# Performance work log

Measured on AMD Instinct MI355X. Metric: run time of the kernel, lower is better.

## Reference

```python
import jax, jax.numpy as jnp
import numpy as np

B, H, T, D = 2, 16, 2048, 64


def setup_inputs() -> dict:
    key = jax.random.key(0)
    kq, kk, kv, km = jax.random.split(key, 4)
    q = jax.random.normal(kq, (B, H, T, D), dtype=jnp.float32)
    k = jax.random.normal(kk, (B, H, T, D), dtype=jnp.float32)
    v = jax.random.normal(kv, (B, H, T, D), dtype=jnp.float32)
    # boolean mask, True = masked out (broadcast over batch and heads)
    mask = jax.random.randint(km, (1, 1, T, T), 0, 2).astype(jnp.bool_)
    return {"q": q, "k": k, "v": v, "mask": mask}


def reference(q, k, v, mask):
    scale = q.shape[-1] ** (-0.5)
    # [B,H,T,T] score matrix (materialized, as in the original)
    scores = jnp.einsum("bhqd,bhkd->bhqk", q, k) * scale
    scores = jnp.where(mask, jnp.float32(-10000.0), scores)
    attn = jax.nn.softmax(scores, axis=-1)
    attn = jnp.where(mask, jnp.float32(0.0), attn)
    return jnp.einsum("bhqk,bhkd->bhqd", attn, v)
```

## Files before the change

### kernel.cpp

```cpp
#include <hip/hip_runtime.h>
#include <hip/hip_bf16.h>

typedef __bf16 bf16x8 __attribute__((ext_vector_type(8)));
typedef __bf16 bf16x4 __attribute__((ext_vector_type(4)));
typedef float  f32x4  __attribute__((ext_vector_type(4)));

#define T_SEQ 2048
#define D_HEAD 64
#define BH_N 32
#define NT_TILES (T_SEQ / 64)
#define QT_N 16
#define IMG_BYTES 16384
#define SCALE_LOG2 0.18033688011112042f

#define WS_IMG ((size_t)0)
#define WS_MB  ((size_t)16u << 20)

static __device__ __forceinline__ f32x4 mfma32(bf16x8 a, bf16x8 b, f32x4 c) {
    return __builtin_amdgcn_mfma_f32_16x16x32_bf16(a, b, c, 0, 0, 0);
}

static __device__ __forceinline__ float fast_exp2(float x) {
#if __has_builtin(__builtin_amdgcn_exp2f)
    return __builtin_amdgcn_exp2f(x);
#else
    return exp2f(x);
#endif
}

static __device__ __forceinline__ void gload16(const void* g, void* l, int lane) {
#if __has_builtin(__builtin_amdgcn_global_load_lds)
    (void)lane;
    __builtin_amdgcn_global_load_lds(
        (const __attribute__((address_space(1))) void*)g,
        (__attribute__((address_space(3))) void*)l, 16, 0, 0);
#else
    *((f32x4*)l + lane) = *(const f32x4*)g;
#endif
}


__global__ __launch_bounds__(256) void prep_kv(const float* __restrict__ k,
                                               const float* __restrict__ v,
                                               char* __restrict__ img) {
    __shared__ __bf16 t[64][72];
    const int bh = blockIdx.y, tt = blockIdx.x, tid = threadIdx.x;
    char* ob = img + ((size_t)bh * NT_TILES + tt) * IMG_BYTES;
    {
        const int kr = tid >> 2, qd = tid & 3, ke = kr & 7;
        const size_t base = ((size_t)bh * T_SEQ + tt * 64 + kr) * D_HEAD + qd * 16;
        const float4 a0 = *(const float4*)(k + base);
        const float4 a1 = *(const float4*)(k + base + 4);
        const float4 a2 = *(const float4*)(k + base + 8);
        const float4 a3 = *(const float4*)(k + base + 12);
        bf16x8 w0, w1;
        w0[0]=(__bf16)a0.x; w0[1]=(__bf16)a0.y; w0[2]=(__bf16)a0.z; w0[3]=(__bf16)a0.w;
        w0[4]=(__bf16)a1.x; w0[5]=(__bf16)a1.y; w0[6]=(__bf16)a1.z; w0[7]=(__bf16)a1.w;
        w1[0]=(__bf16)a2.x; w1[1]=(__bf16)a2.y; w1[2]=(__bf16)a2.z; w1[3]=(__bf16)a2.w;
        w1[4]=(__bf16)a3.x; w1[5]=(__bf16)a3.y; w1[6]=(__bf16)a3.z; w1[7]=(__bf16)a3.w;
        *(bf16x8*)(ob + kr * 128 + (((2 * qd + 0) ^ ke) << 4)) = w0;
        *(bf16x8*)(ob + kr * 128 + (((2 * qd + 1) ^ ke) << 4)) = w1;
    }
    {
        const int tr = tid >> 4, c4 = (tid & 15) * 4;
        const float* src = v + ((size_t)bh * T_SEQ + tt * 64) * D_HEAD;
#pragma unroll
        for (int p = 0; p < 4; ++p) {
            const int row = p * 16 + tr;
            const float4 f = *(const float4*)(src + row * D_HEAD + c4);
            t[c4+0][row] = (__bf16)f.x; t[c4+1][row] = (__bf16)f.y;
            t[c4+2][row] = (__bf16)f.z; t[c4+3][row] = (__bf16)f.w;
        }
        __syncthreads();
        const int d = tid >> 2;
        char* vb = ob + 8192 + d * 128;
#pragma unroll
        for (int mi = 0; mi < 2; ++mi) {
            const int m  = (tid & 3) * 2 + mi;
            const int u  = m ^ (d & 7);
            const int k0 = (u & 1) * 32 + (u >> 1) * 4;
            const bf16x4 lo = *(const bf16x4*)&t[d][k0];
            const bf16x4 hi = *(const bf16x4*)&t[d][k0 + 16];
            *(bf16x8*)(vb + m * 16) = __builtin_shufflevector(lo, hi, 0,1,2,3,4,5,6,7);
        }
    }
}

__global__ void mpack(const int* __restrict__ m, unsigned* __restrict__ nbt) {
    const int i = blockIdx.x * 256 + threadIdx.x;
    const unsigned long long b = __ballot(m[i] != 0);
    if ((threadIdx.x & 63) == 0) {
        const int wi  = i >> 6;
        const int row = wi >> 5;
        const int t   = wi & 31;
        nbt[(size_t)(t * 2 + 0) * 2048 + row] = ~(unsigned)b;
        nbt[(size_t)(t * 2 + 1) * 2048 + row] = ~(unsigned)(b >> 32);
    }
}


__global__ __launch_bounds__(512, 4) void attn15(
    const float* __restrict__ q, const char* __restrict__ img,
    const unsigned* __restrict__ nbt, float* __restrict__ out)
{
    const int l   = blockIdx.x;
    const int m_  = l >> 3;
    const int bh  = ((l & 7) << 2) | (m_ & 3);
    const int qt  = m_ >> 2;

    const int tid = threadIdx.x, wave = tid >> 6, lane = tid & 63;
    const int g = lane >> 4, ln = lane & 15;
    const int qp = wave & 3, kh = wave >> 2;
    const int g4 = g * 4;

    __shared__ __align__(16) char smem[33280];
    float* Ep = (float*)smem;
    float* Os = (float*)(smem + 32768);

    const int qw = qt * 128 + qp * 32;

    bf16x8 qf[2][2];
#pragma unroll
    for (int qs = 0; qs < 2; ++qs) {
        const float* qpt = q + ((size_t)bh * T_SEQ + qw + qs * 16 + ln) * D_HEAD + g * 8;
#pragma unroll
        for (int kc = 0; kc < 2; ++kc) {
            const float4 f0 = *(const float4*)(qpt + kc * 32);
            const float4 f1 = *(const float4*)(qpt + kc * 32 + 4);
            qf[qs][kc][0]=(__bf16)(f0.x*SCALE_LOG2); qf[qs][kc][1]=(__bf16)(f0.y*SCALE_LOG2);
            qf[qs][kc][2]=(__bf16)(f0.z*SCALE_LOG2); qf[qs][kc][3]=(__bf16)(f0.w*SCALE_LOG2);
            qf[qs][kc][4]=(__bf16)(f1.x*SCALE_LOG2); qf[qs][kc][5]=(__bf16)(f1.y*SCALE_LOG2);
            qf[qs][kc][6]=(__bf16)(f1.z*SCALE_LOG2); qf[qs][kc][7]=(__bf16)(f1.w*SCALE_LOG2);
        }
    }

    f32x4 o[2][4];
#pragma unroll
    for (int qs = 0; qs < 2; ++qs)
#pragma unroll
        for (int mt = 0; mt < 4; ++mt) o[qs][mt] = (f32x4){0.f, 0.f, 0.f, 0.f};
    f32x4 osum[2] = { (f32x4){0.f,0.f,0.f,0.f}, (f32x4){0.f,0.f,0.f,0.f} };
    const bf16x8 ones8 = { (__bf16)1.0f, (__bf16)1.0f, (__bf16)1.0f, (__bf16)1.0f,
                           (__bf16)1.0f, (__bf16)1.0f, (__bf16)1.0f, (__bf16)1.0f };
    const f32x4 z4 = (f32x4){0.f, 0.f, 0.f, 0.f};

    const char* ibase = img + (size_t)bh * (NT_TILES * (size_t)IMG_BYTES);
    const unsigned* nb_base = nbt + (size_t)kh * 2048 + qw;

    int koffs[2][2];
#pragma unroll
    for (int ntl = 0; ntl < 2; ++ntl) {
        const int row = (2 * kh + ntl) * 16 + ln;
        const int rb = row * 128 + ((g ^ (ln & 7)) << 4);
        koffs[ntl][0] = rb; koffs[ntl][1] = rb ^ 64;
    }
    int voffs[4];
#pragma unroll
    for (int mt = 0; mt < 4; ++mt)
        voffs[mt] = (mt * 16 + ln) * 128 + ((((g << 1) | kh) ^ (ln & 7)) << 4);

    char* buf0 = smem;
    char* buf1 = smem + 16384;

    auto stage = [&](int tile, char* dstbase) {
        const char* src = ibase + (size_t)tile * IMG_BYTES + wave * 2048 + lane * 16;
        char* dst = dstbase + wave * 2048;
        gload16(src, dst, lane);
        gload16(src + 1024, dst + 1024, lane);
    };

    auto compute_tile = [&](const char* KB, const char* VB, unsigned nw0, unsigned nw1) {
        const unsigned nbs0 = nw0 >> g4;
        const unsigned nbs1 = nw1 >> g4;

        bf16x8 ka[2][2];
#pragma unroll
        for (int ntl = 0; ntl < 2; ++ntl) {
            ka[ntl][0] = *(const bf16x8*)(KB + koffs[ntl][0]);
            ka[ntl][1] = *(const bf16x8*)(KB + koffs[ntl][1]);
        }

        bf16x8 pa8[2];
#pragma unroll
        for (int ntl = 0; ntl < 2; ++ntl) {
#pragma unroll
            for (int qs = 0; qs < 2; ++qs) {
                __builtin_amdgcn_s_setprio(1);
                f32x4 c = mfma32(ka[ntl][0], qf[qs][0], z4);
                c = mfma32(ka[ntl][1], qf[qs][1], c);
                __builtin_amdgcn_s_setprio(0);
                const unsigned nbs = qs ? nbs1 : nbs0;
#pragma unroll
                for (int r = 0; r < 4; ++r) {
                    const float e = fast_exp2(c[r]);
                    const int keep = (int)(nbs << (31 - (ntl * 16 + r))) >> 31;
                    const float p = __builtin_bit_cast(float,
                        __builtin_bit_cast(unsigned, e) & (unsigned)keep);
                    pa8[qs][ntl * 4 + r] = (__bf16)p;
                }
            }
        }

        bf16x8 vv[4];
#pragma unroll
        for (int mt = 0; mt < 4; ++mt) vv[mt] = *(const bf16x8*)(VB + voffs[mt]);
        __builtin_amdgcn_s_setprio(1);
#pragma unroll
        for (int qs = 0; qs < 2; ++qs) osum[qs] = mfma32(pa8[qs], ones8, osum[qs]);
#pragma unroll
        for (int mt = 0; mt < 4; ++mt)
#pragma unroll
            for (int qs = 0; qs < 2; ++qs)
                o[qs][mt] = mfma32(pa8[qs], vv[mt], o[qs][mt]);
        __builtin_amdgcn_s_setprio(0);
    };

    stage(0, buf0);
    unsigned mwA0 = nb_base[ln], mwA1 = nb_base[16 + ln];
    __syncthreads();

#pragma unroll 1
    for (int i = 0; i < NT_TILES / 2; ++i) {
        const int t = 2 * i;
        stage(t + 1, buf1);
        const unsigned* pB = nb_base + (size_t)(t + 1) * 4096;
        const unsigned mwB0 = pB[ln], mwB1 = pB[16 + ln];
        compute_tile(buf0, buf0 + 8192, mwA0, mwA1);
        __syncthreads();
        if (i < NT_TILES / 2 - 1) {
            stage(t + 2, buf0);
            const unsigned* pA = nb_base + (size_t)(t + 2) * 4096;
            mwA0 = pA[ln]; mwA1 = pA[16 + ln];
        }
        compute_tile(buf1, buf1 + 8192, mwB0, mwB1);
        __syncthreads();
    }

#pragma unroll
    for (int pass = 0; pass < 2; ++pass) {
        if ((qp >> 1) == pass) {
            const int qpl = qp & 1;
#pragma unroll
            for (int qs = 0; qs < 2; ++qs) {
#pragma unroll
                for (int mt = 0; mt < 4; ++mt)
#pragma unroll
                    for (int r = 0; r < 4; ++r)
                        Ep[(size_t)kh * 4096 + (qpl * 32 + qs * 16 + g * 4 + r) * 64 + mt * 16 + ln] = o[qs][mt][r];
                if (ln == 0) {
#pragma unroll
                    for (int r = 0; r < 4; ++r)
                        Os[kh * 64 + qpl * 32 + qs * 16 + g * 4 + r] = osum[qs][r];
                }
            }
        }
        __syncthreads();
#pragma unroll
        for (int p2 = 0; p2 < 2; ++p2) {
            const int idx = p2 * 512 + tid;
            const int row = idx >> 4, c4 = (idx & 15) * 4;
            const float sl = Os[row] + Os[64 + row];
            const float inv = (sl > 0.f) ? (1.f / sl) : 0.f;
            const float4 a  = *(const float4*)(Ep + row * 64 + c4);
            const float4 b4 = *(const float4*)(Ep + 4096 + row * 64 + c4);
            const float4 st = { (a.x + b4.x) * inv, (a.y + b4.y) * inv,
                                (a.z + b4.z) * inv, (a.w + b4.w) * inv };
            *(float4*)(out + ((size_t)bh * T_SEQ + qt * 128 + pass * 64 + row) * D_HEAD + c4) = st;
        }
        if (pass == 0) __syncthreads();
    }
}

extern "C" void kernel_launch(void* const* d_in, const int* in_sizes, int n_in,
                              void* d_out, int out_size, void* d_ws, size_t ws_size,
                              hipStream_t stream) {
    const float* q    = (const float*)d_in[0];
    const float* k    = (const float*)d_in[1];
    const float* v    = (const float*)d_in[2];
    const int*   mask = (const int*)d_in[3];
    float*       out  = (float*)d_out;

    char* img = (char*)d_ws + WS_IMG;
    unsigned* nbt = (unsigned*)((char*)d_ws + WS_MB);

    prep_kv<<<dim3(NT_TILES, BH_N), 256, 0, stream>>>(k, v, img);
    mpack<<<(T_SEQ * T_SEQ) / 256, 256, 0, stream>>>(mask, nbt);
    attn15<<<dim3(QT_N * BH_N), 512, 0, stream>>>(q, img, nbt, out);
}
```

Baseline: 155.6 us.

## Quad-buffer K/V tiles in LDS with two tiles per barrier

Expands the LDS staging from two to four K/V tile buffers so prefetch runs two tiles ahead, and halves the number of block-wide barriers per tile. The loop is restructured into groups of four tiles with an explicit epilogue. It also replaces the shift-based mask bit extraction with a signed bitfield extract intrinsic. The doubled LDS footprint reduces how many blocks can reside per CU.

```diff
diff --git a/kernel.cpp b/kernel.cpp
--- a/kernel.cpp
+++ b/kernel.cpp
@@ -25,6 +25,14 @@
     return __builtin_amdgcn_exp2f(x);
 #else
     return exp2f(x);
+#endif
+}
+
+static __device__ __forceinline__ int sext_bit(unsigned w, int idx) {
+#if __has_builtin(__builtin_amdgcn_sbfe)
+    return __builtin_amdgcn_sbfe((int)w, idx, 1);
+#else
+    return (int)(w << (31 - idx)) >> 31;
 #endif
 }
 
@@ -99,7 +107,7 @@
 }
 
 
-__global__ __launch_bounds__(512, 4) void attn15(
+__global__ __launch_bounds__(512, 4) void attn16(
     const float* __restrict__ q, const char* __restrict__ img,
     const unsigned* __restrict__ nbt, float* __restrict__ out)
 {
@@ -113,9 +121,9 @@
     const int qp = wave & 3, kh = wave >> 2;
     const int g4 = g * 4;
 
-    __shared__ __align__(16) char smem[33280];
+    __shared__ __align__(16) char smem[66048];
     float* Ep = (float*)smem;
-    float* Os = (float*)(smem + 32768);
+    float* Os = (float*)(smem + 65536);
 
     const int qw = qt * 128 + qp * 32;
 
@@ -159,8 +167,10 @@
     for (int mt = 0; mt < 4; ++mt)
         voffs[mt] = (mt * 16 + ln) * 128 + ((((g << 1) | kh) ^ (ln & 7)) << 4);
 
-    char* buf0 = smem;
-    char* buf1 = smem + 16384;
+    char* const b0 = smem;
+    char* const b1 = smem + 16384;
+    char* const b2 = smem + 32768;
+    char* const b3 = smem + 49152;
 
     auto stage = [&](int tile, char* dstbase) {
         const char* src = ibase + (size_t)tile * IMG_BYTES + wave * 2048 + lane * 16;
@@ -169,7 +179,8 @@
         gload16(src + 1024, dst + 1024, lane);
     };
 
-    auto compute_tile = [&](const char* KB, const char* VB, unsigned nw0, unsigned nw1) {
+    auto compute_tile = [&](const char* KB, unsigned nw0, unsigned nw1) {
+        const char* VB = KB + 8192;
         const unsigned nbs0 = nw0 >> g4;
         const unsigned nbs1 = nw1 >> g4;
 
@@ -193,7 +204,7 @@
 #pragma unroll
                 for (int r = 0; r < 4; ++r) {
                     const float e = fast_exp2(c[r]);
-                    const int keep = (int)(nbs << (31 - (ntl * 16 + r))) >> 31;
+                    const int keep = sext_bit(nbs, ntl * 16 + r);
                     const float p = __builtin_bit_cast(float,
                         __builtin_bit_cast(unsigned, e) & (unsigned)keep);
                     pa8[qs][ntl * 4 + r] = (__bf16)p;
@@ -215,25 +226,64 @@
         __builtin_amdgcn_s_setprio(0);
     };
 
-    stage(0, buf0);
-    unsigned mwA0 = nb_base[ln], mwA1 = nb_base[16 + ln];
+    unsigned mwA0, mwA1, mwB0, mwB1;
+
+    stage(0, b0);
+    stage(1, b1);
+    mwA0 = nb_base[ln]; mwA1 = nb_base[16 + ln];
     __syncthreads();
 
 #pragma unroll 1
-    for (int i = 0; i < NT_TILES / 2; ++i) {
-        const int t = 2 * i;
-        stage(t + 1, buf1);
-        const unsigned* pB = nb_base + (size_t)(t + 1) * 4096;
-        const unsigned mwB0 = pB[ln], mwB1 = pB[16 + ln];
-        compute_tile(buf0, buf0 + 8192, mwA0, mwA1);
+    for (int i = 0; i < 7; ++i) {
+        const int t = 4 * i;
+        {
+            stage(t + 2, b2);
+            const unsigned* p = nb_base + (size_t)(t + 1) * 4096;
+            mwB0 = p[ln]; mwB1 = p[16 + ln];
+            compute_tile(b0, mwA0, mwA1);
+        }
+        {
+            stage(t + 3, b3);
+            const unsigned* p = nb_base + (size_t)(t + 2) * 4096;
+            mwA0 = p[ln]; mwA1 = p[16 + ln];
+            compute_tile(b1, mwB0, mwB1);
+        }
         __syncthreads();
-        if (i < NT_TILES / 2 - 1) {
-            stage(t + 2, buf0);
-            const unsigned* pA = nb_base + (size_t)(t + 2) * 4096;
-            mwA0 = pA[ln]; mwA1 = pA[16 + ln];
-        }
-        compute_tile(buf1, buf1 + 8192, mwB0, mwB1);
+        {
+            stage(t + 4, b0);
+            const unsigned* p = nb_base + (size_t)(t + 3) * 4096;
+            mwB0 = p[ln]; mwB1 = p[16 + ln];
+            compute_tile(b2, mwA0, mwA1);
+        }
+        {
+            stage(t + 5, b1);
+            const unsigned* p = nb_base + (size_t)(t + 4) * 4096;
+            mwA0 = p[ln]; mwA1 = p[16 + ln];
+            compute_tile(b3, mwB0, mwB1);
+        }
         __syncthreads();
+    }
+
+    {
+        stage(30, b2);
+        const unsigned* p = nb_base + (size_t)29 * 4096;
+        mwB0 = p[ln]; mwB1 = p[16 + ln];
+        compute_tile(b0, mwA0, mwA1);
+    }
+    {
+        stage(31, b3);
+        const unsigned* p = nb_base + (size_t)30 * 4096;
+        mwA0 = p[ln]; mwA1 = p[16 + ln];
+        compute_tile(b1, mwB0, mwB1);
+    }
+    __syncthreads();
+    {
+        const unsigned* p = nb_base + (size_t)31 * 4096;
+        mwB0 = p[ln]; mwB1 = p[16 + ln];
+        compute_tile(b2, mwA0, mwA1);
+    }
+    {
+        compute_tile(b3, mwB0, mwB1);
     }
 
 #pragma unroll
@@ -285,5 +335,5 @@
 
     prep_kv<<<dim3(NT_TILES, BH_N), 256, 0, stream>>>(k, v, img);
     mpack<<<(T_SEQ * T_SEQ) / 256, 256, 0, stream>>>(mask, nbt);
-    attn15<<<dim3(QT_N * BH_N), 512, 0, stream>>>(q, img, nbt, out);
-}
+    attn16<<<dim3(QT_N * BH_N), 512, 0, stream>>>(q, img, nbt, out);
+}
```

Measured after the change: 153.5 us, median of 2. About the same (-1.3%).

## Double per-wave query tile and deepen K/V LDS prefetch to an eight-buffer ring

Applied to the files above, without the earlier changes.

Each wave now handles 64 query rows instead of 32, so every staged K/V tile feeds twice as many MFMAs, and the grid shrinks to 256 workgroups. The two-buffer double-buffering is replaced by an eight-slot LDS ring that prefetches six tiles ahead, with one barrier per pair of tiles, to hide global-load latency. Mask bit extraction uses a signed bitfield-extract builtin. In exchange, LDS use grows to about 130 KB per block and register pressure roughly doubles, which limits occupancy to about one block per CU and halves the number of blocks available to spread across the GPU.

```diff
diff --git a/kernel.cpp b/kernel.cpp
--- a/kernel.cpp
+++ b/kernel.cpp
@@ -9,7 +9,7 @@
 #define D_HEAD 64
 #define BH_N 32
 #define NT_TILES (T_SEQ / 64)
-#define QT_N 16
+#define QT_N 8
 #define IMG_BYTES 16384
 #define SCALE_LOG2 0.18033688011112042f
 
@@ -25,6 +25,14 @@
     return __builtin_amdgcn_exp2f(x);
 #else
     return exp2f(x);
+#endif
+}
+
+static __device__ __forceinline__ int sext_bit(unsigned w, int idx) {
+#if __has_builtin(__builtin_amdgcn_sbfe)
+    return __builtin_amdgcn_sbfe((int)w, idx, 1);
+#else
+    return (int)(w << (31 - idx)) >> 31;
 #endif
 }
 
@@ -99,29 +107,28 @@
 }
 
 
-__global__ __launch_bounds__(512, 4) void attn15(
+__global__ __launch_bounds__(512, 2) void attn18(
     const float* __restrict__ q, const char* __restrict__ img,
     const unsigned* __restrict__ nbt, float* __restrict__ out)
 {
     const int l   = blockIdx.x;
-    const int m_  = l >> 3;
-    const int bh  = ((l & 7) << 2) | (m_ & 3);
-    const int qt  = m_ >> 2;
+    const int bh  = ((l & 7) << 2) | ((l >> 3) & 3);
+    const int qt  = l >> 5;
 
     const int tid = threadIdx.x, wave = tid >> 6, lane = tid & 63;
     const int g = lane >> 4, ln = lane & 15;
     const int qp = wave & 3, kh = wave >> 2;
     const int g4 = g * 4;
 
-    __shared__ __align__(16) char smem[33280];
+    __shared__ __align__(16) char smem[133120];
     float* Ep = (float*)smem;
-    float* Os = (float*)(smem + 32768);
-
-    const int qw = qt * 128 + qp * 32;
-
-    bf16x8 qf[2][2];
-#pragma unroll
-    for (int qs = 0; qs < 2; ++qs) {
+    float* Os = (float*)(smem + 131072);
+
+    const int qw = qt * 256 + qp * 64;
+
+    bf16x8 qf[4][2];
+#pragma unroll
+    for (int qs = 0; qs < 4; ++qs) {
         const float* qpt = q + ((size_t)bh * T_SEQ + qw + qs * 16 + ln) * D_HEAD + g * 8;
 #pragma unroll
         for (int kc = 0; kc < 2; ++kc) {
@@ -134,12 +141,13 @@
         }
     }
 
-    f32x4 o[2][4];
-#pragma unroll
-    for (int qs = 0; qs < 2; ++qs)
+    f32x4 o[4][4];
+#pragma unroll
+    for (int qs = 0; qs < 4; ++qs)
 #pragma unroll
         for (int mt = 0; mt < 4; ++mt) o[qs][mt] = (f32x4){0.f, 0.f, 0.f, 0.f};
-    f32x4 osum[2] = { (f32x4){0.f,0.f,0.f,0.f}, (f32x4){0.f,0.f,0.f,0.f} };
+    f32x4 osum[4] = { (f32x4){0.f,0.f,0.f,0.f}, (f32x4){0.f,0.f,0.f,0.f},
+                      (f32x4){0.f,0.f,0.f,0.f}, (f32x4){0.f,0.f,0.f,0.f} };
     const bf16x8 ones8 = { (__bf16)1.0f, (__bf16)1.0f, (__bf16)1.0f, (__bf16)1.0f,
                            (__bf16)1.0f, (__bf16)1.0f, (__bf16)1.0f, (__bf16)1.0f };
     const f32x4 z4 = (f32x4){0.f, 0.f, 0.f, 0.f};
@@ -159,8 +167,10 @@
     for (int mt = 0; mt < 4; ++mt)
         voffs[mt] = (mt * 16 + ln) * 128 + ((((g << 1) | kh) ^ (ln & 7)) << 4);
 
-    char* buf0 = smem;
-    char* buf1 = smem + 16384;
+    char* const b0 = smem;              char* const b1 = smem + 16384;
+    char* const b2 = smem + 32768;      char* const b3 = smem + 49152;
+    char* const b4 = smem + 65536;      char* const b5 = smem + 81920;
+    char* const b6 = smem + 98304;      char* const b7 = smem + 114688;
 
     auto stage = [&](int tile, char* dstbase) {
         const char* src = ibase + (size_t)tile * IMG_BYTES + wave * 2048 + lane * 16;
@@ -169,9 +179,11 @@
         gload16(src + 1024, dst + 1024, lane);
     };
 
-    auto compute_tile = [&](const char* KB, const char* VB, unsigned nw0, unsigned nw1) {
-        const unsigned nbs0 = nw0 >> g4;
-        const unsigned nbs1 = nw1 >> g4;
+    auto compute_tile = [&](const char* KB, const unsigned* nw) {
+        const char* VB = KB + 8192;
+        unsigned nbs[4];
+#pragma unroll
+        for (int qs = 0; qs < 4; ++qs) nbs[qs] = nw[qs] >> g4;
 
         bf16x8 ka[2][2];
 #pragma unroll
@@ -180,20 +192,23 @@
             ka[ntl][1] = *(const bf16x8*)(KB + koffs[ntl][1]);
         }
 
-        bf16x8 pa8[2];
+        bf16x8 pa8[4];
 #pragma unroll
         for (int ntl = 0; ntl < 2; ++ntl) {
-#pragma unroll
-            for (int qs = 0; qs < 2; ++qs) {
-                __builtin_amdgcn_s_setprio(1);
-                f32x4 c = mfma32(ka[ntl][0], qf[qs][0], z4);
-                c = mfma32(ka[ntl][1], qf[qs][1], c);
-                __builtin_amdgcn_s_setprio(0);
-                const unsigned nbs = qs ? nbs1 : nbs0;
+            f32x4 c[4];
+            __builtin_amdgcn_s_setprio(1);
+#pragma unroll
+            for (int qs = 0; qs < 4; ++qs) {
+                c[qs] = mfma32(ka[ntl][0], qf[qs][0], z4);
+                c[qs] = mfma32(ka[ntl][1], qf[qs][1], c[qs]);
+            }
+            __builtin_amdgcn_s_setprio(0);
+#pragma unroll
+            for (int qs = 0; qs < 4; ++qs) {
 #pragma unroll
                 for (int r = 0; r < 4; ++r) {
-                    const float e = fast_exp2(c[r]);
-                    const int keep = (int)(nbs << (31 - (ntl * 16 + r))) >> 31;
+                    const float e = fast_exp2(c[qs][r]);
+                    const int keep = sext_bit(nbs[qs], ntl * 16 + r);
                     const float p = __builtin_bit_cast(float,
                         __builtin_bit_cast(unsigned, e) & (unsigned)keep);
                     pa8[qs][ntl * 4 + r] = (__bf16)p;
@@ -206,34 +221,38 @@
         for (int mt = 0; mt < 4; ++mt) vv[mt] = *(const bf16x8*)(VB + voffs[mt]);
         __builtin_amdgcn_s_setprio(1);
 #pragma unroll
-        for (int qs = 0; qs < 2; ++qs) osum[qs] = mfma32(pa8[qs], ones8, osum[qs]);
+        for (int qs = 0; qs < 4; ++qs) osum[qs] = mfma32(pa8[qs], ones8, osum[qs]);
 #pragma unroll
         for (int mt = 0; mt < 4; ++mt)
 #pragma unroll
-            for (int qs = 0; qs < 2; ++qs)
+            for (int qs = 0; qs < 4; ++qs)
                 o[qs][mt] = mfma32(pa8[qs], vv[mt], o[qs][mt]);
         __builtin_amdgcn_s_setprio(0);
     };
 
-    stage(0, buf0);
-    unsigned mwA0 = nb_base[ln], mwA1 = nb_base[16 + ln];
+    auto window = [&](const char* X, const char* Y, int t, char* SX, char* SY) {
+        if (t + 6 < NT_TILES) { stage(t + 6, SX); stage(t + 7, SY); }
+        const unsigned* p0 = nb_base + (size_t)t * 4096;
+        const unsigned* p1 = p0 + 4096;
+        unsigned nw0[4], nw1[4];
+#pragma unroll
+        for (int qs = 0; qs < 4; ++qs) { nw0[qs] = p0[qs * 16 + ln]; nw1[qs] = p1[qs * 16 + ln]; }
+        compute_tile(X, nw0);
+        compute_tile(Y, nw1);
+        __syncthreads();
+    };
+
+    stage(0, b0); stage(1, b1); stage(2, b2);
+    stage(3, b3); stage(4, b4); stage(5, b5);
     __syncthreads();
 
 #pragma unroll 1
-    for (int i = 0; i < NT_TILES / 2; ++i) {
-        const int t = 2 * i;
-        stage(t + 1, buf1);
-        const unsigned* pB = nb_base + (size_t)(t + 1) * 4096;
-        const unsigned mwB0 = pB[ln], mwB1 = pB[16 + ln];
-        compute_tile(buf0, buf0 + 8192, mwA0, mwA1);
-        __syncthreads();
-        if (i < NT_TILES / 2 - 1) {
-            stage(t + 2, buf0);
-            const unsigned* pA = nb_base + (size_t)(t + 2) * 4096;
-            mwA0 = pA[ln]; mwA1 = pA[16 + ln];
-        }
-        compute_tile(buf1, buf1 + 8192, mwB0, mwB1);
-        __syncthreads();
+    for (int i = 0; i < 4; ++i) {
+        const int t = 8 * i;
+        window(b0, b1, t,     b6, b7);
+        window(b2, b3, t + 2, b0, b1);
+        window(b4, b5, t + 4, b2, b3);
+        window(b6, b7, t + 6, b4, b5);
     }
 
 #pragma unroll
@@ -241,31 +260,31 @@
         if ((qp >> 1) == pass) {
             const int qpl = qp & 1;
 #pragma unroll
-            for (int qs = 0; qs < 2; ++qs) {
+            for (int qs = 0; qs < 4; ++qs) {
 #pragma unroll
                 for (int mt = 0; mt < 4; ++mt)
 #pragma unroll
                     for (int r = 0; r < 4; ++r)
-                        Ep[(size_t)kh * 4096 + (qpl * 32 + qs * 16 + g * 4 + r) * 64 + mt * 16 + ln] = o[qs][mt][r];
+                        Ep[(size_t)kh * 8192 + (qpl * 64 + qs * 16 + g * 4 + r) * 64 + mt * 16 + ln] = o[qs][mt][r];
                 if (ln == 0) {
 #pragma unroll
                     for (int r = 0; r < 4; ++r)
-                        Os[kh * 64 + qpl * 32 + qs * 16 + g * 4 + r] = osum[qs][r];
+                        Os[kh * 128 + qpl * 64 + qs * 16 + g * 4 + r] = osum[qs][r];
                 }
             }
         }
         __syncthreads();
 #pragma unroll
-        for (int p2 = 0; p2 < 2; ++p2) {
+        for (int p2 = 0; p2 < 4; ++p2) {
             const int idx = p2 * 512 + tid;
             const int row = idx >> 4, c4 = (idx & 15) * 4;
-            const float sl = Os[row] + Os[64 + row];
+            const float sl = Os[row] + Os[128 + row];
             const float inv = (sl > 0.f) ? (1.f / sl) : 0.f;
             const float4 a  = *(const float4*)(Ep + row * 64 + c4);
-            const float4 b4 = *(const float4*)(Ep + 4096 + row * 64 + c4);
-            const float4 st = { (a.x + b4.x) * inv, (a.y + b4.y) * inv,
-                                (a.z + b4.z) * inv, (a.w + b4.w) * inv };
-            *(float4*)(out + ((size_t)bh * T_SEQ + qt * 128 + pass * 64 + row) * D_HEAD + c4) = st;
+            const float4 b4v = *(const float4*)(Ep + 8192 + row * 64 + c4);
+            const float4 st = { (a.x + b4v.x) * inv, (a.y + b4v.y) * inv,
+                                (a.z + b4v.z) * inv, (a.w + b4v.w) * inv };
+            *(float4*)(out + ((size_t)bh * T_SEQ + qt * 256 + pass * 128 + row) * D_HEAD + c4) = st;
         }
         if (pass == 0) __syncthreads();
     }
@@ -285,5 +304,5 @@
 
     prep_kv<<<dim3(NT_TILES, BH_N), 256, 0, stream>>>(k, v, img);
     mpack<<<(T_SEQ * T_SEQ) / 256, 256, 0, stream>>>(mask, nbt);
-    attn15<<<dim3(QT_N * BH_N), 512, 0, stream>>>(q, img, nbt, out);
-}
+    attn18<<<dim3(QT_N * BH_N), 512, 0, stream>>>(q, img, nbt, out);
+}
```

New measurement: 163.3 us. 4.9% more time.
